# Performance work log

Measured on AMD Instinct MI355X. Metric: run time of the kernel, lower is better.

Reference implementation:

```python
import jax, jax.numpy as jnp
import numpy as np

N = 50000       # nodes
E_RND = 750000  # random edges (plus N self-loops)
IN = 512        # in_dim
HID = 64        # hidden_dim
H = 4           # num_heads
L = 2           # blk_size
OUT = 64        # out_dim
NEG = 0.01      # leaky_relu slope (torch default)
ATT_NEG = 0.2   # attention leaky_relu slope (GAT convention)


def setup_inputs() -> dict:
    key = jax.random.key(0)
    ks = jax.random.split(key, 12)
    sl = jnp.arange(N, dtype=jnp.int32)
    src = jnp.concatenate([jax.random.randint(ks[0], (E_RND,), 0, N, dtype=jnp.int32), sl])
    dst = jnp.concatenate([jax.random.randint(ks[1], (E_RND,), 0, N, dtype=jnp.int32), sl])
    ft = jax.random.normal(ks[2], (N, IN), jnp.float32)
    s = lambda f: np.float32(1.0 / np.sqrt(f))
    Wp = jax.random.normal(ks[3], (IN, HID), jnp.float32) * s(IN)
    We = jax.random.normal(ks[4], (HID, HID), jnp.float32) * s(HID)
    a_l = jax.random.normal(ks[5], (L, H, HID), jnp.float32) * s(HID)
    a_r = jax.random.normal(ks[6], (L, H, HID), jnp.float32) * s(HID)
    Wv = jax.random.normal(ks[7], (L, H, HID, HID), jnp.float32) * s(HID)
    Wg_pool = jax.random.normal(ks[8], (L, HID, HID), jnp.float32) * s(HID)
    Wgate = jax.random.normal(ks[9], (L, 3 * HID, H), jnp.float32) * s(3 * HID)
    bgate = jnp.zeros((L, H), jnp.float32)
    Wtran = jax.random.normal(ks[10], (HID * (H + 1), OUT), jnp.float32) * s(HID * (H + 1))
    btran = jnp.zeros((OUT,), jnp.float32)
    return dict(ft=ft, Wp=Wp, We=We, a_l=a_l, a_r=a_r, Wv=Wv, Wg_pool=Wg_pool,
                Wgate=Wgate, bgate=bgate, Wtran=Wtran, btran=btran, src=src, dst=dst)


def _segment_softmax(e, seg, n):
    m = jax.ops.segment_max(e, seg, num_segments=n)
    ex = jnp.exp(e - m[seg])
    s = jax.ops.segment_sum(ex, seg, num_segments=n)
    return ex / s[seg]


def reference(ft, Wp, We, a_l, a_r, Wv, Wg_pool, Wgate, bgate, Wtran, btran, src, dst):
    proj_feat = ft @ Wp                       # [N,HID]
    deg = jax.ops.segment_sum(jnp.ones_like(dst, jnp.float32), dst, num_segments=N)  # [N]
    cur = proj_feat
    for i in range(L):
        proj_z = cur @ We                     # [N,HID] shared attention embedding
        # per-head additive attention logits
        el = jnp.einsum('nd,hd->nh', proj_z, a_l[i])
        er = jnp.einsum('nd,hd->nh', proj_z, a_r[i])
        e = jax.nn.leaky_relu(el[src] + er[dst], ATT_NEG)        # [E,H]
        alpha = _segment_softmax(e, dst, N)                      # [E,H]
        vals = jnp.einsum('nd,hdo->nho', cur, Wv[i])             # [N,H,HID]
        msg = alpha[:, :, None] * vals[src]                      # [E,H,HID]
        agg = jax.ops.segment_sum(msg, dst, num_segments=N)      # [N,H,HID]
        # GaAN gate: [v_i, max-pool of projected neighbor v, mean of neighbor v]
        pooled = cur @ Wg_pool[i]                                # [N,HID]
        mx = jax.ops.segment_max(pooled[src], dst, num_segments=N)
        mn = jax.ops.segment_sum(cur[src], dst, num_segments=N) / deg[:, None]
        gate_in = jnp.concatenate([cur, mx, mn], axis=-1)        # [N,3*HID]
        g = jax.nn.sigmoid(gate_in @ Wgate[i] + bgate[i])        # [N,H]
        agg = agg * g[:, :, None]
        merged = agg.mean(axis=1) if i < L - 1 else agg.reshape(N, H * HID)
        cur = jax.nn.leaky_relu(merged, NEG)
    h = jnp.concatenate([proj_feat, cur], axis=-1)               # [N,HID*(H+1)]
    return h @ Wtran + btran                                     # [N,OUT]
```

## Files before the change

### kernel.cpp

```cpp
#include <hip/hip_runtime.h>

#define NN 50000
#define EE 800000
#define IND 512
#define HD 64
#define NB_SCAN 49

__device__ __forceinline__ float lrelu(float x, float s){ return x > 0.f ? x : s*x; }

__global__ void k_deg(const int* __restrict__ dst, int* __restrict__ deg){
  int e = blockIdx.x*256 + threadIdx.x;
  if(e < EE) atomicAdd(&deg[dst[e]], 1);
}

__global__ void k_scan1(const int* __restrict__ deg, int* __restrict__ psum){
  __shared__ int sh[256];
  int base = blockIdx.x*1024 + threadIdx.x*4;
  int s = 0;
  #pragma unroll
  for(int j=0;j<4;j++){ int i=base+j; if(i<NN) s += deg[i]; }
  sh[threadIdx.x]=s; __syncthreads();
  for(int st=128; st>0; st>>=1){ if(threadIdx.x<st) sh[threadIdx.x]+=sh[threadIdx.x+st]; __syncthreads(); }
  if(threadIdx.x==0) psum[blockIdx.x]=sh[0];
}

__global__ void k_scan2(int* __restrict__ psum, int nb){
  if(threadIdx.x==0){ int acc=0; for(int i=0;i<nb;i++){ int v=psum[i]; psum[i]=acc; acc+=v; } psum[nb]=acc; }
}

__global__ void k_scan3(const int* __restrict__ deg, const int* __restrict__ psum, int* __restrict__ rowp){
  __shared__ int sh[256];
  int t = threadIdx.x;
  int base = blockIdx.x*1024 + t*4;
  int v[4]; int s=0;
  #pragma unroll
  for(int j=0;j<4;j++){ int i=base+j; v[j] = (i<NN)?deg[i]:0; s+=v[j]; }
  sh[t]=s; __syncthreads();
  for(int st=1; st<256; st<<=1){
    int add = (t>=st)? sh[t-st] : 0;
    __syncthreads();
    sh[t] += add;
    __syncthreads();
  }
  int excl = sh[t]-s + psum[blockIdx.x];
  #pragma unroll
  for(int j=0;j<4;j++){ int i=base+j; if(i<NN){ rowp[i]=excl; excl+=v[j]; } }
  if(blockIdx.x==0 && t==0) rowp[NN] = psum[NB_SCAN];
}

__global__ void k_fill(const int* __restrict__ src, const int* __restrict__ dst,
                       const int* __restrict__ rowp, int* __restrict__ cnt, int* __restrict__ csrc){
  int e = blockIdx.x*256 + threadIdx.x;
  if(e < EE){
    int d = dst[e];
    int p = atomicAdd(&cnt[d], 1);
    csrc[rowp[d] + p] = src[e];
  }
}

__device__ __forceinline__ void load_A_tile(const float* __restrict__ A, int row0, int lda, int kcol0, float* As){
  int t = threadIdx.x;
  int lr = t>>2;
  int lc = (t&3)*16;
  float4 a0,a1,a2,a3;
  int row = row0 + lr;
  if(row < NN){
    const float* ap = A + (size_t)row*lda + kcol0 + lc;
    a0=*(const float4*)ap; a1=*(const float4*)(ap+4); a2=*(const float4*)(ap+8); a3=*(const float4*)(ap+12);
  } else {
    a0=a1=a2=a3=make_float4(0.f,0.f,0.f,0.f);
  }
  float* d = As + (size_t)lc*68 + lr;
  d[0*68]=a0.x;  d[1*68]=a0.y;  d[2*68]=a0.z;  d[3*68]=a0.w;
  d[4*68]=a1.x;  d[5*68]=a1.y;  d[6*68]=a1.z;  d[7*68]=a1.w;
  d[8*68]=a2.x;  d[9*68]=a2.y;  d[10*68]=a2.z; d[11*68]=a2.w;
  d[12*68]=a3.x; d[13*68]=a3.y; d[14*68]=a3.z; d[15*68]=a3.w;
}

__device__ __forceinline__ void load_B_tile(const float* __restrict__ B, int krow0, float* Bs){
  int t = threadIdx.x;
  int bk = t>>2; int lc = (t&3)*16;
  const float* bp = B + (size_t)(krow0+bk)*64 + lc;
  *(float4*)(Bs + bk*64 + lc)      = *(const float4*)bp;
  *(float4*)(Bs + bk*64 + lc + 4)  = *(const float4*)(bp+4);
  *(float4*)(Bs + bk*64 + lc + 8)  = *(const float4*)(bp+8);
  *(float4*)(Bs + bk*64 + lc + 12) = *(const float4*)(bp+12);
}

__device__ __forceinline__ void tile64_compute(const float* __restrict__ As, const float* __restrict__ Bs,
                                               float acc[4][4], int ty, int tx){
  #pragma unroll 4
  for(int kk=0; kk<64; kk++){
    float4 a = *(const float4*)(As + kk*68 + ty*4);
    float4 b = *(const float4*)(Bs + kk*64 + tx*4);
    acc[0][0]+=a.x*b.x; acc[0][1]+=a.x*b.y; acc[0][2]+=a.x*b.z; acc[0][3]+=a.x*b.w;
    acc[1][0]+=a.y*b.x; acc[1][1]+=a.y*b.y; acc[1][2]+=a.y*b.z; acc[1][3]+=a.y*b.w;
    acc[2][0]+=a.z*b.x; acc[2][1]+=a.z*b.y; acc[2][2]+=a.z*b.z; acc[2][3]+=a.z*b.w;
    acc[3][0]+=a.w*b.x; acc[3][1]+=a.w*b.y; acc[3][2]+=a.w*b.z; acc[3][3]+=a.w*b.w;
  }
}

__global__ __launch_bounds__(256, 4) void k_gemm_proj(const float* __restrict__ A, const float* __restrict__ B, float* __restrict__ C){
  __shared__ float As[64*68];
  __shared__ float Bs[64*64];
  int row0 = blockIdx.x*64;
  int ty = threadIdx.x>>4, tx = threadIdx.x&15;
  float acc[4][4] = {};
  #pragma unroll 1
  for(int kt=0; kt<IND; kt+=64){
    __syncthreads();
    load_A_tile(A, row0, IND, kt, As);
    load_B_tile(B, kt, Bs);
    __syncthreads();
    tile64_compute(As, Bs, acc, ty, tx);
  }
  #pragma unroll
  for(int i=0;i<4;i++){
    int row = row0 + ty*4 + i;
    if(row < NN) *(float4*)(C + (size_t)row*64 + tx*4) = make_float4(acc[i][0],acc[i][1],acc[i][2],acc[i][3]);
  }
}

__global__ __launch_bounds__(256, 4) void k_nodemm2(const float* __restrict__ cur, const float* __restrict__ We,
                                                    const float* __restrict__ Wg,
                                                    float* __restrict__ projz, float* __restrict__ pooled){
  __shared__ float As[64*68];
  __shared__ float Bs[64*64];
  int row0 = blockIdx.x*64;
  int ty = threadIdx.x>>4, tx = threadIdx.x&15;
  load_A_tile(cur, row0, 64, 0, As);
  #pragma unroll 1
  for(int bi=0; bi<2; ++bi){
    const float* B = bi ? Wg : We;
    float* C = bi ? pooled : projz;
    __syncthreads();
    load_B_tile(B, 0, Bs);
    __syncthreads();
    float acc[4][4] = {};
    tile64_compute(As, Bs, acc, ty, tx);
    #pragma unroll
    for(int i=0;i<4;i++){
      int row = row0 + ty*4 + i;
      if(row < NN) *(float4*)(C + (size_t)row*64 + tx*4) = make_float4(acc[i][0],acc[i][1],acc[i][2],acc[i][3]);
    }
  }
}

__global__ __launch_bounds__(256) void k_eler(const float* __restrict__ projz, const float* __restrict__ al,
                                              const float* __restrict__ ar, float* __restrict__ el, float* __restrict__ er){
  int wid = threadIdx.x>>6, lane = threadIdx.x&63;
  int n = blockIdx.x*4 + wid;
  if(n >= NN) return;
  float z = projz[(size_t)n*64 + lane];
  #pragma unroll
  for(int h=0; h<4; h++){
    float pl = z*al[h*64+lane];
    float pr = z*ar[h*64+lane];
    #pragma unroll
    for(int st=32; st; st>>=1){ pl += __shfl_xor(pl, st, 64); pr += __shfl_xor(pr, st, 64); }
    if(lane==0){ el[(size_t)n*4+h]=pl; er[(size_t)n*4+h]=pr; }
  }
}

__global__ __launch_bounds__(256) void k_edge(const int* __restrict__ rowp, const int* __restrict__ csrc,
    const float* __restrict__ el, const float* __restrict__ er, const float* __restrict__ cur,
    const float* __restrict__ pooled,
    const float* __restrict__ Wg, const float* __restrict__ bg, float* __restrict__ aggcg)
{
  __shared__ int    ssh[4][64];
  __shared__ float4 xsh[4][64];
  int wid = threadIdx.x>>6, lane = threadIdx.x&63;
  int d = blockIdx.x*4 + wid;
  if(d >= NN) return;
  int e0 = rowp[d], e1 = rowp[d+1];
  float4 erd = *(const float4*)(er + (size_t)d*4);
  float n0=0,n1=0,n2=0,n3=0, den0=0,den1=0,den2=0,den3=0, mn=0, mxp=-1e30f;

  for(int c=e0; c<e1; c+=64){
    int jmax = min(64, e1-c);
    float x0=0.f, x1=0.f, x2=0.f, x3=0.f; int s=0;
    if(lane < jmax){
      s = csrc[c+lane];
      float4 ev = *(const float4*)(el + (size_t)s*4);
      x0 = __expf(lrelu(ev.x+erd.x, 0.2f));
      x1 = __expf(lrelu(ev.y+erd.y, 0.2f));
      x2 = __expf(lrelu(ev.z+erd.z, 0.2f));
      x3 = __expf(lrelu(ev.w+erd.w, 0.2f));
      den0+=x0; den1+=x1; den2+=x2; den3+=x3;
    }
    ssh[wid][lane] = s;
    xsh[wid][lane] = make_float4(x0,x1,x2,x3);
    for(int j=0; j<jmax; ++j){
      int sj = __builtin_amdgcn_readfirstlane(ssh[wid][j]);
      float4 xj = xsh[wid][j];
      const float* cp = cur    + (size_t)sj*64;
      const float* pp = pooled + (size_t)sj*64;
      float cv = cp[lane];
      float pv = pp[lane];
      n0 += xj.x*cv; n1 += xj.y*cv; n2 += xj.z*cv; n3 += xj.w*cv;
      mn += cv;
      mxp = fmaxf(mxp, pv);
    }
  }
  #pragma unroll
  for(int st=32; st; st>>=1){
    den0+=__shfl_xor(den0,st,64); den1+=__shfl_xor(den1,st,64);
    den2+=__shfl_xor(den2,st,64); den3+=__shfl_xor(den3,st,64);
  }
  float cd  = cur[(size_t)d*64 + lane];
  float mnn = mn / (float)(e1-e0);
  float4 w0 = *(const float4*)(Wg + lane*4);
  float4 w1 = *(const float4*)(Wg + (64+lane)*4);
  float4 w2 = *(const float4*)(Wg + (128+lane)*4);
  float g0 = cd*w0.x + mxp*w1.x + mnn*w2.x;
  float g1 = cd*w0.y + mxp*w1.y + mnn*w2.y;
  float g2 = cd*w0.z + mxp*w1.z + mnn*w2.z;
  float g3 = cd*w0.w + mxp*w1.w + mnn*w2.w;
  #pragma unroll
  for(int st=32; st; st>>=1){
    g0+=__shfl_xor(g0,st,64); g1+=__shfl_xor(g1,st,64);
    g2+=__shfl_xor(g2,st,64); g3+=__shfl_xor(g3,st,64);
  }
  g0 = 1.f/(1.f+__expf(-(g0+bg[0])));
  g1 = 1.f/(1.f+__expf(-(g1+bg[1])));
  g2 = 1.f/(1.f+__expf(-(g2+bg[2])));
  g3 = 1.f/(1.f+__expf(-(g3+bg[3])));
  float* od = aggcg + (size_t)d*256;
  od[lane]       = g0 * n0/den0;
  od[64 + lane]  = g1 * n1/den1;
  od[128 + lane] = g2 * n2/den2;
  od[192 + lane] = g3 * n3/den3;
}

__global__ __launch_bounds__(256, 4) void k_post0(const float* __restrict__ A, const float* __restrict__ B, float* __restrict__ C){
  __shared__ float As[64*68];
  __shared__ float Bs[64*64];
  int row0 = blockIdx.x*64;
  int ty = threadIdx.x>>4, tx = threadIdx.x&15;
  float acc[4][4] = {};
  #pragma unroll 1
  for(int kt=0; kt<256; kt+=64){
    __syncthreads();
    load_A_tile(A, row0, 256, kt, As);
    load_B_tile(B, kt, Bs);
    __syncthreads();
    tile64_compute(As, Bs, acc, ty, tx);
  }
  #pragma unroll
  for(int i=0;i<4;i++){
    int row = row0 + ty*4 + i;
    if(row < NN) *(float4*)(C + (size_t)row*64 + tx*4) =
      make_float4(lrelu(0.25f*acc[i][0],0.01f), lrelu(0.25f*acc[i][1],0.01f),
                  lrelu(0.25f*acc[i][2],0.01f), lrelu(0.25f*acc[i][3],0.01f));
  }
}

__global__ __launch_bounds__(256, 4) void k_post1(const float* __restrict__ aggcg, const float* __restrict__ Wv1, float* __restrict__ cur2){
  __shared__ float As[64*68];
  __shared__ float Bs[64*64];
  int row0 = blockIdx.x*64;
  int ty = threadIdx.x>>4, tx = threadIdx.x&15;
  #pragma unroll 1
  for(int h=0; h<4; ++h){
    __syncthreads();
    load_A_tile(aggcg + h*64, row0, 256, 0, As);
    load_B_tile(Wv1 + (size_t)h*4096, 0, Bs);
    __syncthreads();
    float acc[4][4] = {};
    tile64_compute(As, Bs, acc, ty, tx);
    #pragma unroll
    for(int i=0;i<4;i++){
      int row = row0 + ty*4 + i;
      if(row < NN) *(float4*)(cur2 + (size_t)row*256 + h*64 + tx*4) =
        make_float4(lrelu(acc[i][0],0.01f), lrelu(acc[i][1],0.01f),
                    lrelu(acc[i][2],0.01f), lrelu(acc[i][3],0.01f));
    }
  }
}

__global__ __launch_bounds__(256, 4) void k_final(const float* __restrict__ pf, const float* __restrict__ cur2,
                                                  const float* __restrict__ Wt, const float* __restrict__ bt,
                                                  float* __restrict__ C){
  __shared__ float As[64*68];
  __shared__ float Bs[64*64];
  int row0 = blockIdx.x*64;
  int ty = threadIdx.x>>4, tx = threadIdx.x&15;
  float acc[4][4] = {};
  #pragma unroll 1
  for(int kt=0; kt<320; kt+=64){
    __syncthreads();
    if(kt==0) load_A_tile(pf, row0, 64, 0, As);
    else      load_A_tile(cur2, row0, 256, kt-64, As);
    load_B_tile(Wt, kt, Bs);
    __syncthreads();
    tile64_compute(As, Bs, acc, ty, tx);
  }
  float4 bias = *(const float4*)(bt + tx*4);
  #pragma unroll
  for(int i=0;i<4;i++){
    int row = row0 + ty*4 + i;
    if(row < NN){
      *(float4*)(C + (size_t)row*64 + tx*4) =
        make_float4(acc[i][0]+bias.x, acc[i][1]+bias.y, acc[i][2]+bias.z, acc[i][3]+bias.w);
    }
  }
}

extern "C" void kernel_launch(void* const* d_in, const int* in_sizes, int n_in,
                              void* d_out, int out_size, void* d_ws, size_t ws_size,
                              hipStream_t stream) {
  const float* ft    = (const float*)d_in[0];
  const float* Wp    = (const float*)d_in[1];
  const float* We    = (const float*)d_in[2];
  const float* a_l   = (const float*)d_in[3];
  const float* a_r   = (const float*)d_in[4];
  const float* Wv    = (const float*)d_in[5];
  const float* Wgp   = (const float*)d_in[6];
  const float* Wgate = (const float*)d_in[7];
  const float* bgate = (const float*)d_in[8];
  const float* Wtran = (const float*)d_in[9];
  const float* btran = (const float*)d_in[10];
  const int*   src   = (const int*)d_in[11];
  const int*   dst   = (const int*)d_in[12];
  float* out = (float*)d_out;

  char* p = (char*)d_ws;
  auto alloc = [&](size_t bytes)->char* { char* r = p; p += (bytes + 255) & ~(size_t)255; return r; };
  int* deg  = (int*)alloc((size_t)NN*4);
  int* cnt  = (int*)alloc((size_t)NN*4);
  int* rowp = (int*)alloc((size_t)(NN+1)*4);
  int* psum = (int*)alloc(64*4);
  int* csrc = (int*)alloc((size_t)EE*4);
  float* pf    = (float*)alloc((size_t)NN*64*4);
  float* cur1  = (float*)alloc((size_t)NN*64*4);
  float* cur2  = (float*)alloc((size_t)NN*256*4);
  float* elb   = (float*)alloc((size_t)NN*4*4);
  float* erb   = (float*)alloc((size_t)NN*4*4);
  float* pz    = (float*)alloc((size_t)NN*64*4);
  float* pool  = (float*)alloc((size_t)NN*64*4);
  float* aggcg = (float*)alloc((size_t)NN*256*4);

  hipMemsetAsync(deg, 0, (size_t)NN*4, stream);
  hipMemsetAsync(cnt, 0, (size_t)NN*4, stream);
  k_deg<<<(EE+255)/256, 256, 0, stream>>>(dst, deg);
  k_scan1<<<NB_SCAN, 256, 0, stream>>>(deg, psum);
  k_scan2<<<1, 64, 0, stream>>>(psum, NB_SCAN);
  k_scan3<<<NB_SCAN, 256, 0, stream>>>(deg, psum, rowp);
  k_fill<<<(EE+255)/256, 256, 0, stream>>>(src, dst, rowp, cnt, csrc);

  k_gemm_proj<<<(NN+63)/64, 256, 0, stream>>>(ft, Wp, pf);

  int gb = (NN+63)/64;
  k_nodemm2<<<gb, 256, 0, stream>>>(pf, We, Wgp, pz, pool);
  k_eler<<<NN/4, 256, 0, stream>>>(pz, a_l, a_r, elb, erb);
  k_edge<<<NN/4, 256, 0, stream>>>(rowp, csrc, elb, erb, pf, pool, Wgate, bgate, aggcg);
  k_post0<<<gb, 256, 0, stream>>>(aggcg, Wv, cur1);
  k_nodemm2<<<gb, 256, 0, stream>>>(cur1, We, Wgp + 4096, pz, pool);
  k_eler<<<NN/4, 256, 0, stream>>>(pz, a_l + 256, a_r + 256, elb, erb);
  k_edge<<<NN/4, 256, 0, stream>>>(rowp, csrc, elb, erb, cur1, pool, Wgate + 768, bgate + 4, aggcg);
  k_post1<<<gb, 256, 0, stream>>>(aggcg, Wv + 16384, cur2);

  k_final<<<gb, 256, 0, stream>>>(pf, cur2, Wtran, btran, out);
}
```

Before: 645.2 us.

## Fold We into attention vectors, pack cur/pooled as half2, fuse post1 into final GEMM

Precomputes We·a_l and We·a_r, so the attention logits come straight from cur and the proj_z GEMM and its buffer are gone. The gather operand for the edge kernel is packed as fp16 pairs of (cur, pooled), which halves the bytes read per neighbour. The layer-2 Wv projection is fused into the final Wtran GEMM through shared memory, so the cur2 intermediate is never written. Using fp16 for neighbour features lowers precision in the aggregation.

Measured after the change: 632.4 us. -2.0%, faster.

```diff
diff --git a/kernel.cpp b/kernel.cpp
--- a/kernel.cpp
+++ b/kernel.cpp
@@ -1,4 +1,5 @@
 #include <hip/hip_runtime.h>
+#include <hip/hip_fp16.h>
 
 #define NN 50000
 #define EE 800000
@@ -56,6 +57,18 @@
     int p = atomicAdd(&cnt[d], 1);
     csrc[rowp[d] + p] = src[e];
   }
+}
+
+__global__ void k_prew(const float* __restrict__ We, const float* __restrict__ al,
+                       const float* __restrict__ ar, float* __restrict__ w_elr){
+  int t = blockIdx.x*256 + threadIdx.x;
+  if(t >= 1024) return;
+  int layer = t>>9, o = (t>>6)&7, k = t&63;
+  const float* a = (o<4 ? al : ar) + layer*256 + (o&3)*64;
+  const float* w = We + k*64;
+  float s = 0.f;
+  for(int d2=0; d2<64; ++d2) s += w[d2]*a[d2];
+  w_elr[t] = s;
 }
 
 __device__ __forceinline__ void load_A_tile(const float* __restrict__ A, int row0, int lda, int kcol0, float* As){
@@ -121,50 +134,53 @@
   }
 }
 
-__global__ __launch_bounds__(256, 4) void k_nodemm2(const float* __restrict__ cur, const float* __restrict__ We,
-                                                    const float* __restrict__ Wg,
-                                                    float* __restrict__ projz, float* __restrict__ pooled){
+__global__ __launch_bounds__(256, 4) void k_nodemm_pack(const float* __restrict__ cur, const float* __restrict__ Wg,
+                                                        __half2* __restrict__ pack){
   __shared__ float As[64*68];
   __shared__ float Bs[64*64];
   int row0 = blockIdx.x*64;
   int ty = threadIdx.x>>4, tx = threadIdx.x&15;
   load_A_tile(cur, row0, 64, 0, As);
-  #pragma unroll 1
-  for(int bi=0; bi<2; ++bi){
-    const float* B = bi ? Wg : We;
-    float* C = bi ? pooled : projz;
-    __syncthreads();
-    load_B_tile(B, 0, Bs);
-    __syncthreads();
-    float acc[4][4] = {};
-    tile64_compute(As, Bs, acc, ty, tx);
-    #pragma unroll
-    for(int i=0;i<4;i++){
-      int row = row0 + ty*4 + i;
-      if(row < NN) *(float4*)(C + (size_t)row*64 + tx*4) = make_float4(acc[i][0],acc[i][1],acc[i][2],acc[i][3]);
-    }
-  }
-}
-
-__global__ __launch_bounds__(256) void k_eler(const float* __restrict__ projz, const float* __restrict__ al,
-                                              const float* __restrict__ ar, float* __restrict__ el, float* __restrict__ er){
+  load_B_tile(Wg, 0, Bs);
+  __syncthreads();
+  float acc[4][4] = {};
+  tile64_compute(As, Bs, acc, ty, tx);
+  #pragma unroll
+  for(int i=0;i<4;i++){
+    int row = row0 + ty*4 + i;
+    if(row < NN){
+      union { uint4 u; __half2 h[4]; } pk;
+      #pragma unroll
+      for(int j=0;j<4;j++){
+        float cv = As[(tx*4+j)*68 + ty*4 + i];
+        pk.h[j] = __floats2half2_rn(cv, acc[i][j]);
+      }
+      *(uint4*)(pack + (size_t)row*64 + tx*4) = pk.u;
+    }
+  }
+}
+
+__global__ __launch_bounds__(256) void k_eler2(const float* __restrict__ cur, const float* __restrict__ w_elr,
+                                               float* __restrict__ el, float* __restrict__ er){
   int wid = threadIdx.x>>6, lane = threadIdx.x&63;
   int n = blockIdx.x*4 + wid;
   if(n >= NN) return;
-  float z = projz[(size_t)n*64 + lane];
-  #pragma unroll
-  for(int h=0; h<4; h++){
-    float pl = z*al[h*64+lane];
-    float pr = z*ar[h*64+lane];
+  float c = cur[(size_t)n*64 + lane];
+  #pragma unroll
+  for(int o=0; o<8; o++){
+    float p = c * w_elr[o*64 + lane];
     #pragma unroll
-    for(int st=32; st; st>>=1){ pl += __shfl_xor(pl, st, 64); pr += __shfl_xor(pr, st, 64); }
-    if(lane==0){ el[(size_t)n*4+h]=pl; er[(size_t)n*4+h]=pr; }
+    for(int st=32; st; st>>=1) p += __shfl_xor(p, st, 64);
+    if(lane==0){
+      if(o<4) el[(size_t)n*4 + o] = p;
+      else    er[(size_t)n*4 + o-4] = p;
+    }
   }
 }
 
 __global__ __launch_bounds__(256) void k_edge(const int* __restrict__ rowp, const int* __restrict__ csrc,
     const float* __restrict__ el, const float* __restrict__ er, const float* __restrict__ cur,
-    const float* __restrict__ pooled,
+    const __half2* __restrict__ pack,
     const float* __restrict__ Wg, const float* __restrict__ bg, float* __restrict__ aggcg)
 {
   __shared__ int    ssh[4][64];
@@ -193,13 +209,10 @@
     for(int j=0; j<jmax; ++j){
       int sj = __builtin_amdgcn_readfirstlane(ssh[wid][j]);
       float4 xj = xsh[wid][j];
-      const float* cp = cur    + (size_t)sj*64;
-      const float* pp = pooled + (size_t)sj*64;
-      float cv = cp[lane];
-      float pv = pp[lane];
-      n0 += xj.x*cv; n1 += xj.y*cv; n2 += xj.z*cv; n3 += xj.w*cv;
-      mn += cv;
-      mxp = fmaxf(mxp, pv);
+      float2 f = __half22float2(pack[(size_t)sj*64 + lane]);
+      n0 += xj.x*f.x; n1 += xj.y*f.x; n2 += xj.z*f.x; n3 += xj.w*f.x;
+      mn += f.x;
+      mxp = fmaxf(mxp, f.y);
     }
   }
   #pragma unroll
@@ -255,45 +268,35 @@
   }
 }
 
-__global__ __launch_bounds__(256, 4) void k_post1(const float* __restrict__ aggcg, const float* __restrict__ Wv1, float* __restrict__ cur2){
+__global__ __launch_bounds__(256, 4) void k_final2(const float* __restrict__ pf, const float* __restrict__ aggcg,
+                                                   const float* __restrict__ Wv1, const float* __restrict__ Wt,
+                                                   const float* __restrict__ bt, float* __restrict__ C){
   __shared__ float As[64*68];
   __shared__ float Bs[64*64];
   int row0 = blockIdx.x*64;
   int ty = threadIdx.x>>4, tx = threadIdx.x&15;
+  float accF[4][4] = {};
+  load_A_tile(pf, row0, 64, 0, As);
+  load_B_tile(Wt, 0, Bs);
+  __syncthreads();
+  tile64_compute(As, Bs, accF, ty, tx);
   #pragma unroll 1
   for(int h=0; h<4; ++h){
     __syncthreads();
     load_A_tile(aggcg + h*64, row0, 256, 0, As);
     load_B_tile(Wv1 + (size_t)h*4096, 0, Bs);
     __syncthreads();
-    float acc[4][4] = {};
-    tile64_compute(As, Bs, acc, ty, tx);
+    float acc1[4][4] = {};
+    tile64_compute(As, Bs, acc1, ty, tx);
+    __syncthreads();
     #pragma unroll
-    for(int i=0;i<4;i++){
-      int row = row0 + ty*4 + i;
-      if(row < NN) *(float4*)(cur2 + (size_t)row*256 + h*64 + tx*4) =
-        make_float4(lrelu(acc[i][0],0.01f), lrelu(acc[i][1],0.01f),
-                    lrelu(acc[i][2],0.01f), lrelu(acc[i][3],0.01f));
-    }
-  }
-}
-
-__global__ __launch_bounds__(256, 4) void k_final(const float* __restrict__ pf, const float* __restrict__ cur2,
-                                                  const float* __restrict__ Wt, const float* __restrict__ bt,
-                                                  float* __restrict__ C){
-  __shared__ float As[64*68];
-  __shared__ float Bs[64*64];
-  int row0 = blockIdx.x*64;
-  int ty = threadIdx.x>>4, tx = threadIdx.x&15;
-  float acc[4][4] = {};
-  #pragma unroll 1
-  for(int kt=0; kt<320; kt+=64){
-    __syncthreads();
-    if(kt==0) load_A_tile(pf, row0, 64, 0, As);
-    else      load_A_tile(cur2, row0, 256, kt-64, As);
-    load_B_tile(Wt, kt, Bs);
-    __syncthreads();
-    tile64_compute(As, Bs, acc, ty, tx);
+    for(int i=0;i<4;i++)
+      #pragma unroll
+      for(int j=0;j<4;j++)
+        As[(tx*4+j)*68 + ty*4 + i] = lrelu(acc1[i][j], 0.01f);
+    load_B_tile(Wt, 64 + h*64, Bs);
+    __syncthreads();
+    tile64_compute(As, Bs, accF, ty, tx);
   }
   float4 bias = *(const float4*)(bt + tx*4);
   #pragma unroll
@@ -301,7 +304,7 @@
     int row = row0 + ty*4 + i;
     if(row < NN){
       *(float4*)(C + (size_t)row*64 + tx*4) =
-        make_float4(acc[i][0]+bias.x, acc[i][1]+bias.y, acc[i][2]+bias.z, acc[i][3]+bias.w);
+        make_float4(accF[i][0]+bias.x, accF[i][1]+bias.y, accF[i][2]+bias.z, accF[i][3]+bias.w);
     }
   }
 }
@@ -331,14 +334,13 @@
   int* rowp = (int*)alloc((size_t)(NN+1)*4);
   int* psum = (int*)alloc(64*4);
   int* csrc = (int*)alloc((size_t)EE*4);
-  float* pf    = (float*)alloc((size_t)NN*64*4);
-  float* cur1  = (float*)alloc((size_t)NN*64*4);
-  float* cur2  = (float*)alloc((size_t)NN*256*4);
-  float* elb   = (float*)alloc((size_t)NN*4*4);
-  float* erb   = (float*)alloc((size_t)NN*4*4);
-  float* pz    = (float*)alloc((size_t)NN*64*4);
-  float* pool  = (float*)alloc((size_t)NN*64*4);
-  float* aggcg = (float*)alloc((size_t)NN*256*4);
+  float*   pf    = (float*)alloc((size_t)NN*64*4);
+  float*   cur1  = (float*)alloc((size_t)NN*64*4);
+  float*   elb   = (float*)alloc((size_t)NN*4*4);
+  float*   erb   = (float*)alloc((size_t)NN*4*4);
+  __half2* pack  = (__half2*)alloc((size_t)NN*64*4);
+  float*   aggcg = (float*)alloc((size_t)NN*256*4);
+  float*   welr  = (float*)alloc(1024*4);
 
   hipMemsetAsync(deg, 0, (size_t)NN*4, stream);
   hipMemsetAsync(cnt, 0, (size_t)NN*4, stream);
@@ -347,18 +349,17 @@
   k_scan2<<<1, 64, 0, stream>>>(psum, NB_SCAN);
   k_scan3<<<NB_SCAN, 256, 0, stream>>>(deg, psum, rowp);
   k_fill<<<(EE+255)/256, 256, 0, stream>>>(src, dst, rowp, cnt, csrc);
+  k_prew<<<4, 256, 0, stream>>>(We, a_l, a_r, welr);
 
   k_gemm_proj<<<(NN+63)/64, 256, 0, stream>>>(ft, Wp, pf);
 
   int gb = (NN+63)/64;
-  k_nodemm2<<<gb, 256, 0, stream>>>(pf, We, Wgp, pz, pool);
-  k_eler<<<NN/4, 256, 0, stream>>>(pz, a_l, a_r, elb, erb);
-  k_edge<<<NN/4, 256, 0, stream>>>(rowp, csrc, elb, erb, pf, pool, Wgate, bgate, aggcg);
+  k_nodemm_pack<<<gb, 256, 0, stream>>>(pf, Wgp, pack);
+  k_eler2<<<NN/4, 256, 0, stream>>>(pf, welr, elb, erb);
+  k_edge<<<NN/4, 256, 0, stream>>>(rowp, csrc, elb, erb, pf, pack, Wgate, bgate, aggcg);
   k_post0<<<gb, 256, 0, stream>>>(aggcg, Wv, cur1);
-  k_nodemm2<<<gb, 256, 0, stream>>>(cur1, We, Wgp + 4096, pz, pool);
-  k_eler<<<NN/4, 256, 0, stream>>>(pz, a_l + 256, a_r + 256, elb, erb);
-  k_edge<<<NN/4, 256, 0, stream>>>(rowp, csrc, elb, erb, cur1, pool, Wgate + 768, bgate + 4, aggcg);
-  k_post1<<<gb, 256, 0, stream>>>(aggcg, Wv + 16384, cur2);
-
-  k_final<<<gb, 256, 0, stream>>>(pf, cur2, Wtran, btran, out);
-}
+  k_nodemm_pack<<<gb, 256, 0, stream>>>(cur1, Wgp + 4096, pack);
+  k_eler2<<<NN/4, 256, 0, stream>>>(cur1, welr + 512, elb, erb);
+  k_edge<<<NN/4, 256, 0, stream>>>(rowp, csrc, elb, erb, cur1, pack, Wgate + 768, bgate + 4, aggcg);
+  k_final2<<<gb, 256, 0, stream>>>(pf, aggcg, Wv + 16384, Wtran, btran, out);
+}
```
